# Kernel optimization log

Hardware: AMD Instinct MI355X
Metric: run time of the kernel (lower is better)

Reference implementation:

```python
import jax, jax.numpy as jnp
import numpy as np

EPS = 1e-5

def setup_inputs() -> dict:
    key = jax.random.key(0)
    kx, kq, kp = jax.random.split(key, 3)
    B, T, d = 4, 4096, 512
    x = jax.random.normal(kx, (B, T, d), dtype=jnp.float32)
    mask = jnp.tril(jnp.ones((T, T), dtype=jnp.int32))  # causal 0/1 mask
    gamma = jnp.ones((d,), dtype=jnp.float32)
    beta = jnp.zeros((d,), dtype=jnp.float32)
    Wqkv = jax.random.normal(kq, (d, 3 * d), dtype=jnp.float32) / np.sqrt(d)
    Wproj = jax.random.normal(kp, (d, d), dtype=jnp.float32) / np.sqrt(d)
    return {"x": x, "mask": mask, "gamma": gamma, "beta": beta, "Wqkv": Wqkv, "Wproj": Wproj}

def reference(x, mask, gamma, beta, Wqkv, Wproj):
    B, T, C = x.shape
    # LayerNorm over last dim
    mu = jnp.mean(x, axis=-1, keepdims=True)
    var = jnp.mean(jnp.square(x - mu), axis=-1, keepdims=True)
    xn = (x - mu) * jax.lax.rsqrt(var + EPS) * gamma + beta
    # QKV projection (no bias)
    qkv = xn @ Wqkv  # [B,T,3C]
    q, k, v = jnp.split(qkv, 3, axis=-1)
    scale = 1.0 / np.sqrt(C)
    dist = jnp.einsum('btc,bsc->bts', q, k) * scale  # [B,T,T]
    dist = jnp.where(mask[:T, :T] == 0, -jnp.inf, dist)
    attn = jax.nn.softmax(dist, axis=-1)
    out = jnp.einsum('bts,bsc->btc', attn, v)
    return out @ Wproj
```

## Files before the change

kernel.cpp:

```cpp
#include <hip/hip_runtime.h>

typedef short bf16x8 __attribute__((ext_vector_type(8)));
typedef float f32x4 __attribute__((ext_vector_type(4)));

#define AS1 __attribute__((address_space(1)))
#define AS3 __attribute__((address_space(3)))

__device__ __forceinline__ void async16(const void* g, void* l) {
    __builtin_amdgcn_global_load_lds((AS1 unsigned*)(unsigned long long)g,
                                     (AS3 unsigned*)l, 16, 0, 0);
}

__device__ __forceinline__ unsigned short f2bf(float f) {
    unsigned u = __builtin_bit_cast(unsigned, f);
    u += 0x7fffu + ((u >> 16) & 1u);
    return (unsigned short)(u >> 16);
}
__device__ __forceinline__ float bf2f(unsigned short s) {
    unsigned u = ((unsigned)s) << 16;
    return __builtin_bit_cast(float, u);
}

__global__ __launch_bounds__(256) void ln_bf16_kernel(
    const float* __restrict__ x, const float* __restrict__ gamma,
    const float* __restrict__ beta, unsigned short* __restrict__ xn, int nrows)
{
    int row = blockIdx.x * 4 + (threadIdx.x >> 6);
    int lane = threadIdx.x & 63;
    if (row >= nrows) return;
    const float4* xr = (const float4*)(x + (size_t)row * 512);
    float4 a = xr[lane], b = xr[lane + 64];
    float s = a.x + a.y + a.z + a.w + b.x + b.y + b.z + b.w;
    #pragma unroll
    for (int m = 1; m < 64; m <<= 1) s += __shfl_xor(s, m);
    float mu = s * (1.0f / 512.0f);
    float dx[8] = {a.x - mu, a.y - mu, a.z - mu, a.w - mu,
                   b.x - mu, b.y - mu, b.z - mu, b.w - mu};
    float ss = 0.f;
    #pragma unroll
    for (int i = 0; i < 8; ++i) ss += dx[i] * dx[i];
    #pragma unroll
    for (int m = 1; m < 64; m <<= 1) ss += __shfl_xor(ss, m);
    float rstd = rsqrtf(ss * (1.0f / 512.0f) + 1e-5f);
    const float4* gp = (const float4*)gamma;
    const float4* bp = (const float4*)beta;
    float4 g0 = gp[lane], g1 = gp[lane + 64], b0 = bp[lane], b1 = bp[lane + 64];
    float y[8];
    y[0] = dx[0] * rstd * g0.x + b0.x; y[1] = dx[1] * rstd * g0.y + b0.y;
    y[2] = dx[2] * rstd * g0.z + b0.z; y[3] = dx[3] * rstd * g0.w + b0.w;
    y[4] = dx[4] * rstd * g1.x + b1.x; y[5] = dx[5] * rstd * g1.y + b1.y;
    y[6] = dx[6] * rstd * g1.z + b1.z; y[7] = dx[7] * rstd * g1.w + b1.w;
    ushort4* orow = (ushort4*)(xn + (size_t)row * 512);
    orow[lane]      = make_ushort4(f2bf(y[0]), f2bf(y[1]), f2bf(y[2]), f2bf(y[3]));
    orow[lane + 64] = make_ushort4(f2bf(y[4]), f2bf(y[5]), f2bf(y[6]), f2bf(y[7]));
}

__global__ __launch_bounds__(256) void transpose_w(
    const float* __restrict__ in, unsigned short* __restrict__ outT, int R, int Cd)
{
    __shared__ float tile[64][65];
    int r0 = blockIdx.x * 64, c0 = blockIdx.y * 64;
    int lr = threadIdx.x >> 6, lc = threadIdx.x & 63;
    #pragma unroll
    for (int i = 0; i < 16; ++i) {
        int r = i * 4 + lr;
        tile[r][lc] = in[(size_t)(r0 + r) * Cd + c0 + lc];
    }
    __syncthreads();
    #pragma unroll
    for (int i = 0; i < 16; ++i) {
        int r = i * 4 + lr;
        outT[(size_t)(c0 + r) * R + r0 + lc] = f2bf(tile[lc][r]);
    }
}

__global__ __launch_bounds__(256) void gemm_qkv(
    const unsigned short* __restrict__ A, const unsigned short* __restrict__ Bt,
    unsigned short* __restrict__ qkOut, unsigned short* __restrict__ vtp)
{
    __shared__ unsigned short As[128 * 64];
    __shared__ unsigned short Bs[128 * 64];
    const int tid = threadIdx.x;
    const int w = tid >> 6, lane = tid & 63, quad = lane >> 4, l15 = lane & 15;
    const int wm = w >> 1, wn = w & 1;
    const size_t m0 = (size_t)blockIdx.x * 128, n0 = (size_t)blockIdx.y * 128;
    f32x4 zero = {0.f, 0.f, 0.f, 0.f};
    f32x4 acc[4][4];
    #pragma unroll
    for (int i = 0; i < 4; ++i)
        #pragma unroll
        for (int j = 0; j < 4; ++j) acc[i][j] = zero;

    for (int k0 = 0; k0 < 512; k0 += 64) {
        __syncthreads();
        #pragma unroll
        for (int r = 0; r < 4; ++r) {
            int s = r * 256 + w * 64 + lane;
            int row = s >> 3, x = s & 7, g = x ^ (row & 7);
            async16(A + (m0 + row) * 512 + k0 + g * 8,
                    (char*)As + (size_t)(r * 256 + w * 64) * 16);
        }
        #pragma unroll
        for (int r = 0; r < 4; ++r) {
            int s = r * 256 + w * 64 + lane;
            int row = s >> 3, x = s & 7, g = x ^ (row & 7);
            async16(Bt + (n0 + row) * 512 + k0 + g * 8,
                    (char*)Bs + (size_t)(r * 256 + w * 64) * 16);
        }
        __syncthreads();
        #pragma unroll
        for (int ks = 0; ks < 2; ++ks) {
            bf16x8 af[4], bf[4];
            int cc = ks * 4 + quad;
            #pragma unroll
            for (int mt = 0; mt < 4; ++mt) {
                int row = wm * 64 + mt * 16 + l15;
                int x = cc ^ (row & 7);
                af[mt] = *(const bf16x8*)(As + row * 64 + x * 8);
            }
            #pragma unroll
            for (int nt = 0; nt < 4; ++nt) {
                int row = wn * 64 + nt * 16 + l15;
                int x = cc ^ (row & 7);
                bf[nt] = *(const bf16x8*)(Bs + row * 64 + x * 8);
            }
            #pragma unroll
            for (int mt = 0; mt < 4; ++mt)
                #pragma unroll
                for (int nt = 0; nt < 4; ++nt)
                    acc[mt][nt] = __builtin_amdgcn_mfma_f32_16x16x32_bf16(
                        af[mt], bf[nt], acc[mt][nt], 0, 0, 0);
        }
    }
    if (n0 < 1024) {
        #pragma unroll
        for (int mt = 0; mt < 4; ++mt)
            #pragma unroll
            for (int nt = 0; nt < 4; ++nt)
                #pragma unroll
                for (int r = 0; r < 4; ++r) {
                    size_t grow = m0 + wm * 64 + mt * 16 + quad * 4 + r;
                    size_t gcol = n0 + wn * 64 + nt * 16 + l15;
                    qkOut[grow * 1024 + gcol] = f2bf(acc[mt][nt][r]);
                }
    } else {
        const int b = (int)(m0 >> 12);
        const int tb = (int)(m0 & 4095);
        #pragma unroll
        for (int mt = 0; mt < 4; ++mt)
            #pragma unroll
            for (int nt = 0; nt < 4; ++nt)
                #pragma unroll
                for (int r = 0; r < 4; ++r) {
                    int t = tb + wm * 64 + mt * 16 + quad * 4 + r;
                    int vcol = (int)(n0 - 1024) + wn * 64 + nt * 16 + l15;
                    int jt = t >> 5;
                    int x = (t >> 3) & 3;
                    vtp[(size_t)(b * 128 + jt) * 16384
                        + (size_t)(vcol * 4 + x) * 8 + (t & 7)] =
                        f2bf(acc[mt][nt][r]);
                }
    }
}

__global__ __launch_bounds__(256) void gemm_bt(
    const unsigned short* __restrict__ A, const unsigned short* __restrict__ Bt,
    void* __restrict__ Cp, int M, int N, int K, int lda, int ldb, int ldc, int outBf16)
{
    __shared__ unsigned short As[128 * 64];
    __shared__ unsigned short Bs[128 * 64];
    const int tid = threadIdx.x;
    const int w = tid >> 6, lane = tid & 63, quad = lane >> 4, l15 = lane & 15;
    const int wm = w >> 1, wn = w & 1;
    const size_t m0 = (size_t)blockIdx.x * 128, n0 = (size_t)blockIdx.y * 128;
    f32x4 zero = {0.f, 0.f, 0.f, 0.f};
    f32x4 acc[4][4];
    #pragma unroll
    for (int i = 0; i < 4; ++i)
        #pragma unroll
        for (int j = 0; j < 4; ++j) acc[i][j] = zero;

    for (int k0 = 0; k0 < K; k0 += 64) {
        __syncthreads();
        #pragma unroll
        for (int r = 0; r < 4; ++r) {
            int s = r * 256 + w * 64 + lane;
            int row = s >> 3, x = s & 7, g = x ^ (row & 7);
            async16(A + (m0 + row) * lda + k0 + g * 8,
                    (char*)As + (size_t)(r * 256 + w * 64) * 16);
        }
        #pragma unroll
        for (int r = 0; r < 4; ++r) {
            int s = r * 256 + w * 64 + lane;
            int row = s >> 3, x = s & 7, g = x ^ (row & 7);
            async16(Bt + (n0 + row) * ldb + k0 + g * 8,
                    (char*)Bs + (size_t)(r * 256 + w * 64) * 16);
        }
        __syncthreads();
        #pragma unroll
        for (int ks = 0; ks < 2; ++ks) {
            bf16x8 af[4], bf[4];
            int cc = ks * 4 + quad;
            #pragma unroll
            for (int mt = 0; mt < 4; ++mt) {
                int row = wm * 64 + mt * 16 + l15;
                int x = cc ^ (row & 7);
                af[mt] = *(const bf16x8*)(As + row * 64 + x * 8);
            }
            #pragma unroll
            for (int nt = 0; nt < 4; ++nt) {
                int row = wn * 64 + nt * 16 + l15;
                int x = cc ^ (row & 7);
                bf[nt] = *(const bf16x8*)(Bs + row * 64 + x * 8);
            }
            #pragma unroll
            for (int mt = 0; mt < 4; ++mt)
                #pragma unroll
                for (int nt = 0; nt < 4; ++nt)
                    acc[mt][nt] = __builtin_amdgcn_mfma_f32_16x16x32_bf16(
                        af[mt], bf[nt], acc[mt][nt], 0, 0, 0);
        }
    }
    #pragma unroll
    for (int mt = 0; mt < 4; ++mt)
        #pragma unroll
        for (int nt = 0; nt < 4; ++nt)
            #pragma unroll
            for (int r = 0; r < 4; ++r) {
                size_t grow = m0 + wm * 64 + mt * 16 + quad * 4 + r;
                size_t gcol = n0 + wn * 64 + nt * 16 + l15;
                float v = acc[mt][nt][r];
                if (outBf16) ((unsigned short*)Cp)[grow * ldc + gcol] = f2bf(v);
                else         ((float*)Cp)[grow * ldc + gcol] = v;
            }
}

__global__ __launch_bounds__(256, 2) void attn_kernel(
    const unsigned short* __restrict__ qk,
    const unsigned short* __restrict__ vtp,
    unsigned short* __restrict__ ph0, unsigned short* __restrict__ ph1,
    float* __restrict__ lp)
{
    __shared__ unsigned short Ks[2][32 * 512];
    __shared__ unsigned short Ps[64 * 40];

    const int id = blockIdx.x;
    const int cu = id & 255, hi = id >> 8;
    const int b = cu & 3;
    const int q = hi ? (63 - (cu >> 2)) : (cu >> 2);
    const int h = hi;

    const int jt0 = h ? (q + 1) : 0;
    const int jtN = h ? (2 * q + 2) : (q + 1);

    const int tid = threadIdx.x, w = tid >> 6, lane = tid & 63;
    const int quad = lane >> 4, l15 = lane & 15;
    const float scale = 0.04419417382415922f;
    f32x4 zero = {0.f, 0.f, 0.f, 0.f};

    const unsigned short* kbase = qk + (size_t)(b * 4096) * 1024 + 512;
    const unsigned short* vbase = vtp + (size_t)(b * 128) * 16384;
    unsigned short* dst = h ? ph1 : ph0;

    const int gE = (lane & ~7) | ((lane ^ w) & 7);
    const int gO = (lane & ~7) | ((lane ^ (w + 4)) & 7);
    const size_t kOffE = (size_t)w * 1024 + (size_t)gE * 8;
    const size_t kOffO = (size_t)(w + 4) * 1024 + (size_t)gO * 8;
    const size_t vLane = (size_t)w * 4096 + (size_t)l15 * 32 + (size_t)quad * 8;

    bf16x8 qf[16];
    {
        const unsigned short* qb =
            qk + (size_t)(b * 4096 + q * 64 + w * 16 + l15) * 1024;
        #pragma unroll
        for (int ks = 0; ks < 16; ++ks)
            qf[ks] = *(const bf16x8*)(qb + ks * 32 + quad * 8);
    }
    f32x4 o[4][8];
    #pragma unroll
    for (int i = 0; i < 4; ++i)
        #pragma unroll
        for (int d = 0; d < 8; ++d) o[i][d] = zero;
    float li[4] = {0.f, 0.f, 0.f, 0.f};

    #define STAGE_K(BUF, T)                                                      \
    {                                                                            \
        const unsigned short* kg = kbase + (size_t)(T) * 32768;                  \
        _Pragma("unroll")                                                        \
        for (int rr = 0; rr < 4; ++rr) {                                         \
            async16(kg + (size_t)(2 * rr) * 4096 + kOffE,                        \
                    (char*)(&Ks[BUF][0]) + (size_t)((2 * rr) * 256 + w * 64) * 16);\
            async16(kg + (size_t)(2 * rr) * 4096 + kOffO,                        \
                    (char*)(&Ks[BUF][0]) + (size_t)((2 * rr + 1) * 256 + w * 64) * 16);\
        }                                                                        \
    }

    STAGE_K(0, jt0);
    __syncthreads();
    int cur = 0;

    for (int jt = jt0; jt < jtN; ++jt) {
        if (jt + 1 < jtN) STAGE_K(cur ^ 1, jt + 1);

        f32x4 sa[2];
        sa[0] = zero; sa[1] = zero;
        __builtin_amdgcn_s_setprio(1);
        #pragma unroll
        for (int ks = 0; ks < 16; ++ks) {
            int cc = ks * 4 + quad;
            #pragma unroll
            for (int nt = 0; nt < 2; ++nt) {
                int jr = nt * 16 + l15;
                int xg = (cc & ~7) | ((cc ^ jr) & 7);
                bf16x8 kf = *(const bf16x8*)(&Ks[cur][jr * 512 + xg * 8]);
                sa[nt] = __builtin_amdgcn_mfma_f32_16x16x32_bf16(
                    qf[ks], kf, sa[nt], 0, 0, 0);
            }
        }
        __builtin_amdgcn_s_setprio(0);
        const int trow = q * 64 + w * 16 + quad * 4;
        #pragma unroll
        for (int r = 0; r < 4; ++r) {
            #pragma unroll
            for (int nt = 0; nt < 2; ++nt) {
                int col = jt * 32 + nt * 16 + l15;
                float sv = sa[nt][r] * scale;
                float pv = __expf(fminf(sv, 60.f));
                if (col > trow + r) pv = 0.f;
                li[r] += pv;
                Ps[(w * 16 + quad * 4 + r) * 40 + nt * 16 + l15] = f2bf(pv);
            }
        }
        asm volatile("s_waitcnt lgkmcnt(0)" ::: "memory");
        __builtin_amdgcn_s_barrier();

        const unsigned short* vt = vbase + (size_t)jt * 16384 + vLane;
        bf16x8 vfr[8];
        #pragma unroll
        for (int i = 0; i < 8; ++i)
            vfr[i] = *(const bf16x8*)(vt + (size_t)i * 512);
        __builtin_amdgcn_s_setprio(1);
        #pragma unroll
        for (int qi = 0; qi < 4; ++qi) {
            bf16x8 pa = *(const bf16x8*)(Ps + (qi * 16 + l15) * 40 + quad * 8);
            #pragma unroll
            for (int i = 0; i < 8; ++i)
                o[qi][i] = __builtin_amdgcn_mfma_f32_16x16x32_bf16(
                    pa, vfr[i], o[qi][i], 0, 0, 0);
        }
        __builtin_amdgcn_s_setprio(0);
        __syncthreads();
        cur ^= 1;
    }
    #undef STAGE_K

    #pragma unroll
    for (int r = 0; r < 4; ++r) {
        float s = li[r];
        s += __shfl_xor(s, 1);
        s += __shfl_xor(s, 2);
        s += __shfl_xor(s, 4);
        s += __shfl_xor(s, 8);
        if (l15 == 0)
            lp[h * 16384 + b * 4096 + q * 64 + w * 16 + quad * 4 + r] = s;
    }
    unsigned short* ob = dst + (size_t)(b * 4096 + q * 64) * 512 + w * 128;
    #pragma unroll
    for (int qi = 0; qi < 4; ++qi)
        #pragma unroll
        for (int df = 0; df < 8; ++df)
            #pragma unroll
            for (int r = 0; r < 4; ++r)
                ob[(size_t)(qi * 16 + quad * 4 + r) * 512 + df * 16 + l15] =
                    f2bf(o[qi][df][r]);
}

__global__ __launch_bounds__(256) void combine_kernel(
    const unsigned short* __restrict__ ph0, const unsigned short* __restrict__ ph1,
    const float* __restrict__ lp, unsigned short* __restrict__ att)
{
    int t = blockIdx.x * 4 + (threadIdx.x >> 6);
    int lane = threadIdx.x & 63;
    float inv = 1.0f / (lp[t] + lp[16384 + t]);
    const ushort4* pa = (const ushort4*)(ph0 + (size_t)t * 512 + lane * 8);
    const ushort4* pb = (const ushort4*)(ph1 + (size_t)t * 512 + lane * 8);
    ushort4* po = (ushort4*)(att + (size_t)t * 512 + lane * 8);
    #pragma unroll
    for (int i = 0; i < 2; ++i) {
        ushort4 a = pa[i], b = pb[i];
        po[i] = make_ushort4(
            f2bf((bf2f(a.x) + bf2f(b.x)) * inv),
            f2bf((bf2f(a.y) + bf2f(b.y)) * inv),
            f2bf((bf2f(a.z) + bf2f(b.z)) * inv),
            f2bf((bf2f(a.w) + bf2f(b.w)) * inv));
    }
}

extern "C" void kernel_launch(void* const* d_in, const int* in_sizes, int n_in,
                              void* d_out, int out_size, void* d_ws, size_t ws_size,
                              hipStream_t stream)
{
    const float* x     = (const float*)d_in[0];
    const float* gamma = (const float*)d_in[2];
    const float* beta  = (const float*)d_in[3];
    const float* Wqkv  = (const float*)d_in[4];
    const float* Wproj = (const float*)d_in[5];
    float* out = (float*)d_out;

    char* ws = (char*)d_ws;
    unsigned short* qk     = (unsigned short*)(ws);
    unsigned short* ph1    = (unsigned short*)(ws + 33554432);
    unsigned short* vtp    = (unsigned short*)(ws + 50331648);
    unsigned short* xn     = (unsigned short*)(ws + 67108864);
    unsigned short* wqkvT  = (unsigned short*)(ws + 83886080);
    unsigned short* wprojT = (unsigned short*)(ws + 85458944);
    unsigned short* ph0    = xn;
    float*          lp     = (float*)wqkvT;
    unsigned short* att    = vtp;

    ln_bf16_kernel<<<4096, 256, 0, stream>>>(x, gamma, beta, xn, 16384);
    transpose_w<<<dim3(8, 24), 256, 0, stream>>>(Wqkv, wqkvT, 512, 1536);
    transpose_w<<<dim3(8, 8), 256, 0, stream>>>(Wproj, wprojT, 512, 512);
    gemm_qkv<<<dim3(128, 12), 256, 0, stream>>>(xn, wqkvT, qk, vtp);
    attn_kernel<<<512, 256, 0, stream>>>(qk, vtp, ph0, ph1, lp);
    combine_kernel<<<4096, 256, 0, stream>>>(ph0, ph1, lp, att);
    gemm_bt<<<dim3(128, 4), 256, 0, stream>>>(att, wprojT, out,
                                              16384, 512, 512, 512, 512, 512, 0);
}
```

Before: 350.9 us.

## Use 64-wide key tiles in attention and drop K double buffering

Widens the attention key tile from 32 to 64 columns, so each iteration computes four score blocks and two PV k-steps, and halves the loop iteration count. The causal split of work between the two blocks per query tile is rebalanced for the wider tiles. K is now staged into a single buffer with a barrier before and after the load, replacing the prefetch double-buffer. This cuts the number of barriers and loop overheads but exposes K load latency that was previously overlapped, and diagonal tiles do more masked work.

```diff
diff --git a/kernel.cpp b/kernel.cpp
--- a/kernel.cpp
+++ b/kernel.cpp
@@ -241,8 +241,8 @@
     unsigned short* __restrict__ ph0, unsigned short* __restrict__ ph1,
     float* __restrict__ lp)
 {
-    __shared__ unsigned short Ks[2][32 * 512];
-    __shared__ unsigned short Ps[64 * 40];
+    __shared__ unsigned short Ks[64 * 512];
+    __shared__ unsigned short Ps[64 * 72];
 
     const int id = blockIdx.x;
     const int cu = id & 255, hi = id >> 8;
@@ -250,8 +250,9 @@
     const int q = hi ? (63 - (cu >> 2)) : (cu >> 2);
     const int h = hi;
 
-    const int jt0 = h ? (q + 1) : 0;
-    const int jtN = h ? (2 * q + 2) : (q + 1);
+    const int half0 = (q + 2) >> 1;
+    const int jt0 = h ? half0 : 0;
+    const int jtN = h ? (q + 1) : half0;
 
     const int tid = threadIdx.x, w = tid >> 6, lane = tid & 63;
     const int quad = lane >> 4, l15 = lane & 15;
@@ -263,9 +264,8 @@
     unsigned short* dst = h ? ph1 : ph0;
 
     const int gE = (lane & ~7) | ((lane ^ w) & 7);
-    const int gO = (lane & ~7) | ((lane ^ (w + 4)) & 7);
     const size_t kOffE = (size_t)w * 1024 + (size_t)gE * 8;
-    const size_t kOffO = (size_t)(w + 4) * 1024 + (size_t)gO * 8;
+    const size_t kOffO = (size_t)(w + 4) * 1024 + (size_t)(gE ^ 4) * 8;
     const size_t vLane = (size_t)w * 4096 + (size_t)l15 * 32 + (size_t)quad * 8;
 
     bf16x8 qf[16];
@@ -283,36 +283,31 @@
         for (int d = 0; d < 8; ++d) o[i][d] = zero;
     float li[4] = {0.f, 0.f, 0.f, 0.f};
 
-    #define STAGE_K(BUF, T)                                                      \
-    {                                                                            \
-        const unsigned short* kg = kbase + (size_t)(T) * 32768;                  \
-        _Pragma("unroll")                                                        \
-        for (int rr = 0; rr < 4; ++rr) {                                         \
-            async16(kg + (size_t)(2 * rr) * 4096 + kOffE,                        \
-                    (char*)(&Ks[BUF][0]) + (size_t)((2 * rr) * 256 + w * 64) * 16);\
-            async16(kg + (size_t)(2 * rr) * 4096 + kOffO,                        \
-                    (char*)(&Ks[BUF][0]) + (size_t)((2 * rr + 1) * 256 + w * 64) * 16);\
-        }                                                                        \
-    }
-
-    STAGE_K(0, jt0);
-    __syncthreads();
-    int cur = 0;
-
     for (int jt = jt0; jt < jtN; ++jt) {
-        if (jt + 1 < jtN) STAGE_K(cur ^ 1, jt + 1);
-
-        f32x4 sa[2];
-        sa[0] = zero; sa[1] = zero;
+        __syncthreads();
+        {
+            const unsigned short* kg = kbase + (size_t)jt * 65536;
+            #pragma unroll
+            for (int rr = 0; rr < 8; ++rr) {
+                async16(kg + (size_t)(2 * rr) * 4096 + kOffE,
+                        (char*)Ks + (size_t)((2 * rr) * 256 + w * 64) * 16);
+                async16(kg + (size_t)(2 * rr) * 4096 + kOffO,
+                        (char*)Ks + (size_t)((2 * rr + 1) * 256 + w * 64) * 16);
+            }
+        }
+        __syncthreads();
+
+        f32x4 sa[4];
+        sa[0] = zero; sa[1] = zero; sa[2] = zero; sa[3] = zero;
         __builtin_amdgcn_s_setprio(1);
         #pragma unroll
         for (int ks = 0; ks < 16; ++ks) {
             int cc = ks * 4 + quad;
             #pragma unroll
-            for (int nt = 0; nt < 2; ++nt) {
+            for (int nt = 0; nt < 4; ++nt) {
                 int jr = nt * 16 + l15;
                 int xg = (cc & ~7) | ((cc ^ jr) & 7);
-                bf16x8 kf = *(const bf16x8*)(&Ks[cur][jr * 512 + xg * 8]);
+                bf16x8 kf = *(const bf16x8*)(Ks + jr * 512 + xg * 8);
                 sa[nt] = __builtin_amdgcn_mfma_f32_16x16x32_bf16(
                     qf[ks], kf, sa[nt], 0, 0, 0);
             }
@@ -322,37 +317,39 @@
         #pragma unroll
         for (int r = 0; r < 4; ++r) {
             #pragma unroll
-            for (int nt = 0; nt < 2; ++nt) {
-                int col = jt * 32 + nt * 16 + l15;
+            for (int nt = 0; nt < 4; ++nt) {
+                int col = jt * 64 + nt * 16 + l15;
                 float sv = sa[nt][r] * scale;
                 float pv = __expf(fminf(sv, 60.f));
                 if (col > trow + r) pv = 0.f;
                 li[r] += pv;
-                Ps[(w * 16 + quad * 4 + r) * 40 + nt * 16 + l15] = f2bf(pv);
+                Ps[(w * 16 + quad * 4 + r) * 72 + nt * 16 + l15] = f2bf(pv);
             }
         }
         asm volatile("s_waitcnt lgkmcnt(0)" ::: "memory");
         __builtin_amdgcn_s_barrier();
 
-        const unsigned short* vt = vbase + (size_t)jt * 16384 + vLane;
-        bf16x8 vfr[8];
-        #pragma unroll
-        for (int i = 0; i < 8; ++i)
-            vfr[i] = *(const bf16x8*)(vt + (size_t)i * 512);
-        __builtin_amdgcn_s_setprio(1);
-        #pragma unroll
-        for (int qi = 0; qi < 4; ++qi) {
-            bf16x8 pa = *(const bf16x8*)(Ps + (qi * 16 + l15) * 40 + quad * 8);
+        #pragma unroll
+        for (int ks2 = 0; ks2 < 2; ++ks2) {
+            const unsigned short* vt =
+                vbase + (size_t)(2 * jt + ks2) * 16384 + vLane;
+            bf16x8 vfr[8];
             #pragma unroll
             for (int i = 0; i < 8; ++i)
-                o[qi][i] = __builtin_amdgcn_mfma_f32_16x16x32_bf16(
-                    pa, vfr[i], o[qi][i], 0, 0, 0);
-        }
-        __builtin_amdgcn_s_setprio(0);
-        __syncthreads();
-        cur ^= 1;
-    }
-    #undef STAGE_K
+                vfr[i] = *(const bf16x8*)(vt + (size_t)i * 512);
+            __builtin_amdgcn_s_setprio(1);
+            #pragma unroll
+            for (int qi = 0; qi < 4; ++qi) {
+                bf16x8 pa = *(const bf16x8*)(Ps + (qi * 16 + l15) * 72
+                                                + ks2 * 32 + quad * 8);
+                #pragma unroll
+                for (int i = 0; i < 8; ++i)
+                    o[qi][i] = __builtin_amdgcn_mfma_f32_16x16x32_bf16(
+                        pa, vfr[i], o[qi][i], 0, 0, 0);
+            }
+            __builtin_amdgcn_s_setprio(0);
+        }
+    }
 
     #pragma unroll
     for (int r = 0; r < 4; ++r) {
```

After: 357.6 us. Within noise of the previous version (+1.9%).

## Fuse split-attention combine into projection GEMM and merge weight transposes

Applied to the files above, without the earlier changes.

Removes the separate combine kernel. The projection GEMM now loads both partial attention outputs and the two softmax denominators, normalises them, and writes the bf16 A tile to shared memory itself. This avoids writing and re-reading the combined attention tensor and drops one launch. The two weight-transpose launches are also merged into one grid. In exchange, the A tile is loaded synchronously with extra arithmetic instead of through async global-to-LDS loads, and each of the 4 N-blocks repeats the combine work.

```diff
diff --git a/kernel.cpp b/kernel.cpp
--- a/kernel.cpp
+++ b/kernel.cpp
@@ -55,11 +55,19 @@
     orow[lane + 64] = make_ushort4(f2bf(y[4]), f2bf(y[5]), f2bf(y[6]), f2bf(y[7]));
 }
 
-__global__ __launch_bounds__(256) void transpose_w(
-    const float* __restrict__ in, unsigned short* __restrict__ outT, int R, int Cd)
+__global__ __launch_bounds__(256) void transpose_w2(
+    const float* __restrict__ wqkv, const float* __restrict__ wproj,
+    unsigned short* __restrict__ wqkvT, unsigned short* __restrict__ wprojT)
 {
     __shared__ float tile[64][65];
-    int r0 = blockIdx.x * 64, c0 = blockIdx.y * 64;
+    const int R = 512;
+    int by = blockIdx.y;
+    const float* in;
+    unsigned short* outT;
+    int Cd, c0;
+    if (by < 24) { in = wqkv;  outT = wqkvT;  Cd = 1536; c0 = by * 64; }
+    else         { in = wproj; outT = wprojT; Cd = 512;  c0 = (by - 24) * 64; }
+    int r0 = blockIdx.x * 64;
     int lr = threadIdx.x >> 6, lc = threadIdx.x & 63;
     #pragma unroll
     for (int i = 0; i < 16; ++i) {
@@ -163,78 +171,6 @@
     }
 }
 
-__global__ __launch_bounds__(256) void gemm_bt(
-    const unsigned short* __restrict__ A, const unsigned short* __restrict__ Bt,
-    void* __restrict__ Cp, int M, int N, int K, int lda, int ldb, int ldc, int outBf16)
-{
-    __shared__ unsigned short As[128 * 64];
-    __shared__ unsigned short Bs[128 * 64];
-    const int tid = threadIdx.x;
-    const int w = tid >> 6, lane = tid & 63, quad = lane >> 4, l15 = lane & 15;
-    const int wm = w >> 1, wn = w & 1;
-    const size_t m0 = (size_t)blockIdx.x * 128, n0 = (size_t)blockIdx.y * 128;
-    f32x4 zero = {0.f, 0.f, 0.f, 0.f};
-    f32x4 acc[4][4];
-    #pragma unroll
-    for (int i = 0; i < 4; ++i)
-        #pragma unroll
-        for (int j = 0; j < 4; ++j) acc[i][j] = zero;
-
-    for (int k0 = 0; k0 < K; k0 += 64) {
-        __syncthreads();
-        #pragma unroll
-        for (int r = 0; r < 4; ++r) {
-            int s = r * 256 + w * 64 + lane;
-            int row = s >> 3, x = s & 7, g = x ^ (row & 7);
-            async16(A + (m0 + row) * lda + k0 + g * 8,
-                    (char*)As + (size_t)(r * 256 + w * 64) * 16);
-        }
-        #pragma unroll
-        for (int r = 0; r < 4; ++r) {
-            int s = r * 256 + w * 64 + lane;
-            int row = s >> 3, x = s & 7, g = x ^ (row & 7);
-            async16(Bt + (n0 + row) * ldb + k0 + g * 8,
-                    (char*)Bs + (size_t)(r * 256 + w * 64) * 16);
-        }
-        __syncthreads();
-        #pragma unroll
-        for (int ks = 0; ks < 2; ++ks) {
-            bf16x8 af[4], bf[4];
-            int cc = ks * 4 + quad;
-            #pragma unroll
-            for (int mt = 0; mt < 4; ++mt) {
-                int row = wm * 64 + mt * 16 + l15;
-                int x = cc ^ (row & 7);
-                af[mt] = *(const bf16x8*)(As + row * 64 + x * 8);
-            }
-            #pragma unroll
-            for (int nt = 0; nt < 4; ++nt) {
-                int row = wn * 64 + nt * 16 + l15;
-                int x = cc ^ (row & 7);
-                bf[nt] = *(const bf16x8*)(Bs + row * 64 + x * 8);
-            }
-            #pragma unroll
-            for (int mt = 0; mt < 4; ++mt)
-                #pragma unroll
-                for (int nt = 0; nt < 4; ++nt)
-                    acc[mt][nt] = __builtin_amdgcn_mfma_f32_16x16x32_bf16(
-                        af[mt], bf[nt], acc[mt][nt], 0, 0, 0);
-        }
-    }
-    #pragma unroll
-    for (int mt = 0; mt < 4; ++mt)
-        #pragma unroll
-        for (int nt = 0; nt < 4; ++nt)
-            #pragma unroll
-            for (int r = 0; r < 4; ++r) {
-                size_t grow = m0 + wm * 64 + mt * 16 + quad * 4 + r;
-                size_t gcol = n0 + wn * 64 + nt * 16 + l15;
-                float v = acc[mt][nt][r];
-                if (outBf16) ((unsigned short*)Cp)[grow * ldc + gcol] = f2bf(v);
-                else         ((float*)Cp)[grow * ldc + gcol] = v;
-            }
-}
-
 __global__ __launch_bounds__(256, 2) void attn_kernel(
     const unsigned short* __restrict__ qk,
     const unsigned short* __restrict__ vtp,
@@ -375,25 +311,83 @@
                     f2bf(o[qi][df][r]);
 }
 
-__global__ __launch_bounds__(256) void combine_kernel(
+__global__ __launch_bounds__(256) void gemm_proj(
     const unsigned short* __restrict__ ph0, const unsigned short* __restrict__ ph1,
-    const float* __restrict__ lp, unsigned short* __restrict__ att)
-{
-    int t = blockIdx.x * 4 + (threadIdx.x >> 6);
-    int lane = threadIdx.x & 63;
-    float inv = 1.0f / (lp[t] + lp[16384 + t]);
-    const ushort4* pa = (const ushort4*)(ph0 + (size_t)t * 512 + lane * 8);
-    const ushort4* pb = (const ushort4*)(ph1 + (size_t)t * 512 + lane * 8);
-    ushort4* po = (ushort4*)(att + (size_t)t * 512 + lane * 8);
-    #pragma unroll
-    for (int i = 0; i < 2; ++i) {
-        ushort4 a = pa[i], b = pb[i];
-        po[i] = make_ushort4(
-            f2bf((bf2f(a.x) + bf2f(b.x)) * inv),
-            f2bf((bf2f(a.y) + bf2f(b.y)) * inv),
-            f2bf((bf2f(a.z) + bf2f(b.z)) * inv),
-            f2bf((bf2f(a.w) + bf2f(b.w)) * inv));
-    }
+    const float* __restrict__ lp, const unsigned short* __restrict__ Bt,
+    float* __restrict__ out)
+{
+    __shared__ unsigned short As[128 * 64];
+    __shared__ unsigned short Bs[128 * 64];
+    const int tid = threadIdx.x;
+    const int w = tid >> 6, lane = tid & 63, quad = lane >> 4, l15 = lane & 15;
+    const int wm = w >> 1, wn = w & 1;
+    const size_t m0 = (size_t)blockIdx.x * 128, n0 = (size_t)blockIdx.y * 128;
+    f32x4 zero = {0.f, 0.f, 0.f, 0.f};
+    f32x4 acc[4][4];
+    #pragma unroll
+    for (int i = 0; i < 4; ++i)
+        #pragma unroll
+        for (int j = 0; j < 4; ++j) acc[i][j] = zero;
+
+    for (int k0 = 0; k0 < 512; k0 += 64) {
+        __syncthreads();
+        #pragma unroll
+        for (int r = 0; r < 4; ++r) {
+            int s = r * 256 + tid;
+            int row = s >> 3, x = s & 7, g = x ^ (row & 7);
+            size_t t = m0 + row;
+            float inv = 1.0f / (lp[t] + lp[16384 + t]);
+            bf16x8 a = *(const bf16x8*)(ph0 + t * 512 + k0 + g * 8);
+            bf16x8 bb = *(const bf16x8*)(ph1 + t * 512 + k0 + g * 8);
+            bf16x8 v;
+            #pragma unroll
+            for (int e = 0; e < 8; ++e)
+                v[e] = (short)f2bf((bf2f((unsigned short)a[e])
+                                  + bf2f((unsigned short)bb[e])) * inv);
+            *(bf16x8*)(As + (size_t)s * 8) = v;
+        }
+        #pragma unroll
+        for (int r = 0; r < 4; ++r) {
+            int s = r * 256 + w * 64 + lane;
+            int row = s >> 3, x = s & 7, g = x ^ (row & 7);
+            async16(Bt + (n0 + row) * 512 + k0 + g * 8,
+                    (char*)Bs + (size_t)(r * 256 + w * 64) * 16);
+        }
+        __syncthreads();
+        #pragma unroll
+        for (int ks = 0; ks < 2; ++ks) {
+            bf16x8 af[4], bf[4];
+            int cc = ks * 4 + quad;
+            #pragma unroll
+            for (int mt = 0; mt < 4; ++mt) {
+                int row = wm * 64 + mt * 16 + l15;
+                int x = cc ^ (row & 7);
+                af[mt] = *(const bf16x8*)(As + row * 64 + x * 8);
+            }
+            #pragma unroll
+            for (int nt = 0; nt < 4; ++nt) {
+                int row = wn * 64 + nt * 16 + l15;
+                int x = cc ^ (row & 7);
+                bf[nt] = *(const bf16x8*)(Bs + row * 64 + x * 8);
+            }
+            #pragma unroll
+            for (int mt = 0; mt < 4; ++mt)
+                #pragma unroll
+                for (int nt = 0; nt < 4; ++nt)
+                    acc[mt][nt] = __builtin_amdgcn_mfma_f32_16x16x32_bf16(
+                        af[mt], bf[nt], acc[mt][nt], 0, 0, 0);
+        }
+    }
+    #pragma unroll
+    for (int mt = 0; mt < 4; ++mt)
+        #pragma unroll
+        for (int nt = 0; nt < 4; ++nt)
+            #pragma unroll
+            for (int r = 0; r < 4; ++r) {
+                size_t grow = m0 + wm * 64 + mt * 16 + quad * 4 + r;
+                size_t gcol = n0 + wn * 64 + nt * 16 + l15;
+                out[grow * 512 + gcol] = acc[mt][nt][r];
+            }
 }
 
 extern "C" void kernel_launch(void* const* d_in, const int* in_sizes, int n_in,
@@ -416,14 +410,10 @@
     unsigned short* wprojT = (unsigned short*)(ws + 85458944);
     unsigned short* ph0    = xn;
     float*          lp     = (float*)wqkvT;
-    unsigned short* att    = vtp;
 
     ln_bf16_kernel<<<4096, 256, 0, stream>>>(x, gamma, beta, xn, 16384);
-    transpose_w<<<dim3(8, 24), 256, 0, stream>>>(Wqkv, wqkvT, 512, 1536);
-    transpose_w<<<dim3(8, 8), 256, 0, stream>>>(Wproj, wprojT, 512, 512);
+    transpose_w2<<<dim3(8, 32), 256, 0, stream>>>(Wqkv, Wproj, wqkvT, wprojT);
     gemm_qkv<<<dim3(128, 12), 256, 0, stream>>>(xn, wqkvT, qk, vtp);
     attn_kernel<<<512, 256, 0, stream>>>(qk, vtp, ph0, ph1, lp);
-    combine_kernel<<<4096, 256, 0, stream>>>(ph0, ph1, lp, att);
-    gemm_bt<<<dim3(128, 4), 256, 0, stream>>>(att, wprojT, out,
-                                              16384, 512, 512, 512, 512, 512, 0);
-}
+    gemm_proj<<<dim3(128, 4), 256, 0, stream>>>(ph0, ph1, lp, wprojT, out);
+}
```

New measurement: 341.9 us. 1.03x faster.

## Split causal attention KV range into four chunks with paired query tiles

Applied to the files above, without the earlier changes.

The attention kernel now gives each block two query tiles, a short one and a long one mirrored across the sequence, each covering a quarter of its causal KV range. This replaces the previous two-way split, so work per block is more even and per-block latency is shorter. The combine kernel now sums four partial outputs and four row sums, with two extra partial buffers placed in the output buffer before the final GEMM overwrites it. The two weight-transpose launches are also merged into one, which adds extra combine traffic and a second Q load per block.

```diff
diff --git a/kernel.cpp b/kernel.cpp
--- a/kernel.cpp
+++ b/kernel.cpp
@@ -55,11 +55,19 @@
     orow[lane + 64] = make_ushort4(f2bf(y[4]), f2bf(y[5]), f2bf(y[6]), f2bf(y[7]));
 }
 
-__global__ __launch_bounds__(256) void transpose_w(
-    const float* __restrict__ in, unsigned short* __restrict__ outT, int R, int Cd)
+__global__ __launch_bounds__(256) void transpose_w2(
+    const float* __restrict__ wqkv, const float* __restrict__ wproj,
+    unsigned short* __restrict__ wqkvT, unsigned short* __restrict__ wprojT)
 {
     __shared__ float tile[64][65];
-    int r0 = blockIdx.x * 64, c0 = blockIdx.y * 64;
+    const int R = 512;
+    int by = blockIdx.y;
+    const float* in;
+    unsigned short* outT;
+    int Cd, c0;
+    if (by < 24) { in = wqkv;  outT = wqkvT;  Cd = 1536; c0 = by * 64; }
+    else         { in = wproj; outT = wprojT; Cd = 512;  c0 = (by - 24) * 64; }
+    int r0 = blockIdx.x * 64;
     int lr = threadIdx.x >> 6, lc = threadIdx.x & 63;
     #pragma unroll
     for (int i = 0; i < 16; ++i) {
@@ -239,19 +247,14 @@
     const unsigned short* __restrict__ qk,
     const unsigned short* __restrict__ vtp,
     unsigned short* __restrict__ ph0, unsigned short* __restrict__ ph1,
+    unsigned short* __restrict__ ph2, unsigned short* __restrict__ ph3,
     float* __restrict__ lp)
 {
     __shared__ unsigned short Ks[2][32 * 512];
     __shared__ unsigned short Ps[64 * 40];
 
-    const int id = blockIdx.x;
-    const int cu = id & 255, hi = id >> 8;
-    const int b = cu & 3;
-    const int q = hi ? (63 - (cu >> 2)) : (cu >> 2);
-    const int h = hi;
-
-    const int jt0 = h ? (q + 1) : 0;
-    const int jtN = h ? (2 * q + 2) : (q + 1);
+    const int i = blockIdx.x;
+    const int a = i & 63, b = (i >> 6) & 3, j2 = i >> 8;
 
     const int tid = threadIdx.x, w = tid >> 6, lane = tid & 63;
     const int quad = lane >> 4, l15 = lane & 15;
@@ -260,28 +263,12 @@
 
     const unsigned short* kbase = qk + (size_t)(b * 4096) * 1024 + 512;
     const unsigned short* vbase = vtp + (size_t)(b * 128) * 16384;
-    unsigned short* dst = h ? ph1 : ph0;
 
     const int gE = (lane & ~7) | ((lane ^ w) & 7);
     const int gO = (lane & ~7) | ((lane ^ (w + 4)) & 7);
     const size_t kOffE = (size_t)w * 1024 + (size_t)gE * 8;
     const size_t kOffO = (size_t)(w + 4) * 1024 + (size_t)gO * 8;
     const size_t vLane = (size_t)w * 4096 + (size_t)l15 * 32 + (size_t)quad * 8;
-
-    bf16x8 qf[16];
-    {
-        const unsigned short* qb =
-            qk + (size_t)(b * 4096 + q * 64 + w * 16 + l15) * 1024;
-        #pragma unroll
-        for (int ks = 0; ks < 16; ++ks)
-            qf[ks] = *(const bf16x8*)(qb + ks * 32 + quad * 8);
-    }
-    f32x4 o[4][8];
-    #pragma unroll
-    for (int i = 0; i < 4; ++i)
-        #pragma unroll
-        for (int d = 0; d < 8; ++d) o[i][d] = zero;
-    float li[4] = {0.f, 0.f, 0.f, 0.f};
 
     #define STAGE_K(BUF, T)                                                      \
     {                                                                            \
@@ -295,104 +282,134 @@
         }                                                                        \
     }
 
-    STAGE_K(0, jt0);
-    __syncthreads();
-    int cur = 0;
-
-    for (int jt = jt0; jt < jtN; ++jt) {
-        if (jt + 1 < jtN) STAGE_K(cur ^ 1, jt + 1);
-
-        f32x4 sa[2];
-        sa[0] = zero; sa[1] = zero;
-        __builtin_amdgcn_s_setprio(1);
-        #pragma unroll
-        for (int ks = 0; ks < 16; ++ks) {
-            int cc = ks * 4 + quad;
-            #pragma unroll
-            for (int nt = 0; nt < 2; ++nt) {
-                int jr = nt * 16 + l15;
-                int xg = (cc & ~7) | ((cc ^ jr) & 7);
-                bf16x8 kf = *(const bf16x8*)(&Ks[cur][jr * 512 + xg * 8]);
-                sa[nt] = __builtin_amdgcn_mfma_f32_16x16x32_bf16(
-                    qf[ks], kf, sa[nt], 0, 0, 0);
-            }
-        }
-        __builtin_amdgcn_s_setprio(0);
-        const int trow = q * 64 + w * 16 + quad * 4;
+    #pragma unroll 1
+    for (int s = 0; s < 2; ++s) {
+        const int q = s ? (63 - a) : a;
+        const int j = s ? (j2 + 2) : j2;
+        const int T2 = 2 * q + 2;
+        const int t0 = (j * T2) >> 2;
+        const int t1 = ((j + 1) * T2) >> 2;
+
+        bf16x8 qf[16];
+        {
+            const unsigned short* qb =
+                qk + (size_t)(b * 4096 + q * 64 + w * 16 + l15) * 1024;
+            #pragma unroll
+            for (int ks = 0; ks < 16; ++ks)
+                qf[ks] = *(const bf16x8*)(qb + ks * 32 + quad * 8);
+        }
+        f32x4 o[4][8];
+        #pragma unroll
+        for (int ii = 0; ii < 4; ++ii)
+            #pragma unroll
+            for (int d = 0; d < 8; ++d) o[ii][d] = zero;
+        float li[4] = {0.f, 0.f, 0.f, 0.f};
+
+        STAGE_K(0, t0);
+        __syncthreads();
+        int cur = 0;
+
+        #pragma unroll 1
+        for (int jt = t0; jt < t1; ++jt) {
+            if (jt + 1 < t1) STAGE_K(cur ^ 1, jt + 1);
+
+            f32x4 sa[2];
+            sa[0] = zero; sa[1] = zero;
+            __builtin_amdgcn_s_setprio(1);
+            #pragma unroll
+            for (int ks = 0; ks < 16; ++ks) {
+                int cc = ks * 4 + quad;
+                #pragma unroll
+                for (int nt = 0; nt < 2; ++nt) {
+                    int jr = nt * 16 + l15;
+                    int xg = (cc & ~7) | ((cc ^ jr) & 7);
+                    bf16x8 kf = *(const bf16x8*)(&Ks[cur][jr * 512 + xg * 8]);
+                    sa[nt] = __builtin_amdgcn_mfma_f32_16x16x32_bf16(
+                        qf[ks], kf, sa[nt], 0, 0, 0);
+                }
+            }
+            __builtin_amdgcn_s_setprio(0);
+            const int trow = q * 64 + w * 16 + quad * 4;
+            #pragma unroll
+            for (int r = 0; r < 4; ++r) {
+                #pragma unroll
+                for (int nt = 0; nt < 2; ++nt) {
+                    int col = jt * 32 + nt * 16 + l15;
+                    float sv = sa[nt][r] * scale;
+                    float pv = __expf(fminf(sv, 60.f));
+                    if (col > trow + r) pv = 0.f;
+                    li[r] += pv;
+                    Ps[(w * 16 + quad * 4 + r) * 40 + nt * 16 + l15] = f2bf(pv);
+                }
+            }
+            asm volatile("s_waitcnt lgkmcnt(0)" ::: "memory");
+            __builtin_amdgcn_s_barrier();
+
+            const unsigned short* vt = vbase + (size_t)jt * 16384 + vLane;
+            bf16x8 vfr[8];
+            #pragma unroll
+            for (int ii = 0; ii < 8; ++ii)
+                vfr[ii] = *(const bf16x8*)(vt + (size_t)ii * 512);
+            __builtin_amdgcn_s_setprio(1);
+            #pragma unroll
+            for (int qi = 0; qi < 4; ++qi) {
+                bf16x8 pa = *(const bf16x8*)(Ps + (qi * 16 + l15) * 40 + quad * 8);
+                #pragma unroll
+                for (int ii = 0; ii < 8; ++ii)
+                    o[qi][ii] = __builtin_amdgcn_mfma_f32_16x16x32_bf16(
+                        pa, vfr[ii], o[qi][ii], 0, 0, 0);
+            }
+            __builtin_amdgcn_s_setprio(0);
+            __syncthreads();
+            cur ^= 1;
+        }
+
+        unsigned short* dst = (j == 0) ? ph0 : (j == 1) ? ph1
+                            : (j == 2) ? ph2 : ph3;
         #pragma unroll
         for (int r = 0; r < 4; ++r) {
-            #pragma unroll
-            for (int nt = 0; nt < 2; ++nt) {
-                int col = jt * 32 + nt * 16 + l15;
-                float sv = sa[nt][r] * scale;
-                float pv = __expf(fminf(sv, 60.f));
-                if (col > trow + r) pv = 0.f;
-                li[r] += pv;
-                Ps[(w * 16 + quad * 4 + r) * 40 + nt * 16 + l15] = f2bf(pv);
-            }
-        }
-        asm volatile("s_waitcnt lgkmcnt(0)" ::: "memory");
-        __builtin_amdgcn_s_barrier();
-
-        const unsigned short* vt = vbase + (size_t)jt * 16384 + vLane;
-        bf16x8 vfr[8];
-        #pragma unroll
-        for (int i = 0; i < 8; ++i)
-            vfr[i] = *(const bf16x8*)(vt + (size_t)i * 512);
-        __builtin_amdgcn_s_setprio(1);
-        #pragma unroll
-        for (int qi = 0; qi < 4; ++qi) {
-            bf16x8 pa = *(const bf16x8*)(Ps + (qi * 16 + l15) * 40 + quad * 8);
-            #pragma unroll
-            for (int i = 0; i < 8; ++i)
-                o[qi][i] = __builtin_amdgcn_mfma_f32_16x16x32_bf16(
-                    pa, vfr[i], o[qi][i], 0, 0, 0);
-        }
-        __builtin_amdgcn_s_setprio(0);
-        __syncthreads();
-        cur ^= 1;
+            float t = li[r];
+            t += __shfl_xor(t, 1);
+            t += __shfl_xor(t, 2);
+            t += __shfl_xor(t, 4);
+            t += __shfl_xor(t, 8);
+            if (l15 == 0)
+                lp[j * 16384 + b * 4096 + q * 64 + w * 16 + quad * 4 + r] = t;
+        }
+        unsigned short* ob = dst + (size_t)(b * 4096 + q * 64) * 512 + w * 128;
+        #pragma unroll
+        for (int qi = 0; qi < 4; ++qi)
+            #pragma unroll
+            for (int df = 0; df < 8; ++df)
+                #pragma unroll
+                for (int r = 0; r < 4; ++r)
+                    ob[(size_t)(qi * 16 + quad * 4 + r) * 512 + df * 16 + l15] =
+                        f2bf(o[qi][df][r]);
     }
     #undef STAGE_K
-
-    #pragma unroll
-    for (int r = 0; r < 4; ++r) {
-        float s = li[r];
-        s += __shfl_xor(s, 1);
-        s += __shfl_xor(s, 2);
-        s += __shfl_xor(s, 4);
-        s += __shfl_xor(s, 8);
-        if (l15 == 0)
-            lp[h * 16384 + b * 4096 + q * 64 + w * 16 + quad * 4 + r] = s;
-    }
-    unsigned short* ob = dst + (size_t)(b * 4096 + q * 64) * 512 + w * 128;
-    #pragma unroll
-    for (int qi = 0; qi < 4; ++qi)
-        #pragma unroll
-        for (int df = 0; df < 8; ++df)
-            #pragma unroll
-            for (int r = 0; r < 4; ++r)
-                ob[(size_t)(qi * 16 + quad * 4 + r) * 512 + df * 16 + l15] =
-                    f2bf(o[qi][df][r]);
 }
 
 __global__ __launch_bounds__(256) void combine_kernel(
     const unsigned short* __restrict__ ph0, const unsigned short* __restrict__ ph1,
+    const unsigned short* __restrict__ ph2, const unsigned short* __restrict__ ph3,
     const float* __restrict__ lp, unsigned short* __restrict__ att)
 {
     int t = blockIdx.x * 4 + (threadIdx.x >> 6);
     int lane = threadIdx.x & 63;
-    float inv = 1.0f / (lp[t] + lp[16384 + t]);
+    float inv = 1.0f / (lp[t] + lp[16384 + t] + lp[32768 + t] + lp[49152 + t]);
     const ushort4* pa = (const ushort4*)(ph0 + (size_t)t * 512 + lane * 8);
     const ushort4* pb = (const ushort4*)(ph1 + (size_t)t * 512 + lane * 8);
+    const ushort4* pc = (const ushort4*)(ph2 + (size_t)t * 512 + lane * 8);
+    const ushort4* pd = (const ushort4*)(ph3 + (size_t)t * 512 + lane * 8);
     ushort4* po = (ushort4*)(att + (size_t)t * 512 + lane * 8);
     #pragma unroll
     for (int i = 0; i < 2; ++i) {
-        ushort4 a = pa[i], b = pb[i];
+        ushort4 a = pa[i], b = pb[i], c = pc[i], d = pd[i];
         po[i] = make_ushort4(
-            f2bf((bf2f(a.x) + bf2f(b.x)) * inv),
-            f2bf((bf2f(a.y) + bf2f(b.y)) * inv),
-            f2bf((bf2f(a.z) + bf2f(b.z)) * inv),
-            f2bf((bf2f(a.w) + bf2f(b.w)) * inv));
+            f2bf((bf2f(a.x) + bf2f(b.x) + bf2f(c.x) + bf2f(d.x)) * inv),
+            f2bf((bf2f(a.y) + bf2f(b.y) + bf2f(c.y) + bf2f(d.y)) * inv),
+            f2bf((bf2f(a.z) + bf2f(b.z) + bf2f(c.z) + bf2f(d.z)) * inv),
+            f2bf((bf2f(a.w) + bf2f(b.w) + bf2f(c.w) + bf2f(d.w)) * inv));
     }
 }
 
@@ -415,15 +432,16 @@
     unsigned short* wqkvT  = (unsigned short*)(ws + 83886080);
     unsigned short* wprojT = (unsigned short*)(ws + 85458944);
     unsigned short* ph0    = xn;
+    unsigned short* ph2    = (unsigned short*)out;
+    unsigned short* ph3    = (unsigned short*)out + (size_t)8388608;
     float*          lp     = (float*)wqkvT;
     unsigned short* att    = vtp;
 
     ln_bf16_kernel<<<4096, 256, 0, stream>>>(x, gamma, beta, xn, 16384);
-    transpose_w<<<dim3(8, 24), 256, 0, stream>>>(Wqkv, wqkvT, 512, 1536);
-    transpose_w<<<dim3(8, 8), 256, 0, stream>>>(Wproj, wprojT, 512, 512);
+    transpose_w2<<<dim3(8, 32), 256, 0, stream>>>(Wqkv, Wproj, wqkvT, wprojT);
     gemm_qkv<<<dim3(128, 12), 256, 0, stream>>>(xn, wqkvT, qk, vtp);
-    attn_kernel<<<512, 256, 0, stream>>>(qk, vtp, ph0, ph1, lp);
-    combine_kernel<<<4096, 256, 0, stream>>>(ph0, ph1, lp, att);
+    attn_kernel<<<512, 256, 0, stream>>>(qk, vtp, ph0, ph1, ph2, ph3, lp);
+    combine_kernel<<<4096, 256, 0, stream>>>(ph0, ph1, ph2, ph3, lp, att);
     gemm_bt<<<dim3(128, 4), 256, 0, stream>>>(att, wprojT, out,
                                               16384, 512, 512, 512, 512, 512, 0);
 }
```

After: 407.2 us. 1.16x slower.
